# Performance work log

Measured on AMD Instinct MI355X. Metric: run time of the kernel, lower is better.

## Reference

```python
import jax, jax.numpy as jnp
import numpy as np


def setup_inputs() -> dict:
    key = jax.random.key(0)
    ks = jax.random.split(key, 9)
    B, Cr, H, W = 16, 1024, 28, 28
    Cs, Hs, Ws = 256, 25, 25  # Hs == Ws so adaptive pool == mean over width
    Ci = 512
    return {
        "x_rgb": jax.random.normal(ks[0], (B, Cr, H, W), jnp.float32),
        "x_skel": jax.random.normal(ks[1], (B, Cs, Hs, Ws), jnp.float32),
        "Wq": jax.random.normal(ks[2], (Ci, Cr), jnp.float32) * (Cr ** -0.5),
        "bq": jax.random.normal(ks[3], (Ci,), jnp.float32) * 0.01,
        "Wk": jax.random.normal(ks[4], (Ci, Cs), jnp.float32) * (Cs ** -0.5),
        "bk": jax.random.normal(ks[5], (Ci,), jnp.float32) * 0.01,
        "Wv": jax.random.normal(ks[6], (Cr, Cs), jnp.float32) * (Cs ** -0.5),
        "bv": jax.random.normal(ks[7], (Cr,), jnp.float32) * 0.01,
        "gamma": jax.random.normal(ks[8], (1,), jnp.float32) * 0.1,
    }


def reference(x_rgb, x_skel, Wq, bq, Wk, bk, Wv, bv, gamma):
    B, Cr, H, W = x_rgb.shape
    Ws = x_skel.shape[3]
    # adaptive_avg_pool2d(x_skel, (Ws, 1)) with Hs == Ws -> mean over width
    pooled = jnp.mean(x_skel, axis=3)  # [B, Cs, Ws]
    # 1x1 conv projections as matmuls
    q = jnp.einsum('ic,bchw->bihw', Wq, x_rgb) + bq[None, :, None, None]
    q = q.reshape(B, -1, H * W).transpose(0, 2, 1)          # [B, HW, Ci]
    k = jnp.einsum('ic,bcs->bis', Wk, pooled) + bk[None, :, None]  # [B, Ci, Ws]
    energy = jnp.einsum('bni,bis->bns', q, k)               # [B, HW, Ws]
    attention = jax.nn.softmax(energy, axis=-1)             # [B, HW, Ws]
    v = jnp.einsum('rc,bcs->brs', Wv, pooled) + bv[None, :, None]  # [B, Cr, Ws]
    out = jnp.einsum('brs,bns->brn', v, attention)          # [B, Cr, HW]
    out = out.reshape(B, Cr, H, W)
    return gamma[0] * out + x_rgb
```

## Files before the change

### kernel.cpp

```cpp
#include <hip/hip_runtime.h>

#define BB 16
#define CR 1024
#define HWD 784
#define HW2 392
#define CS 256
#define SSZ 25
#define SP 28
#define CI 512
#define CSPLIT 8
#define CCHUNK 128
#define RSPLIT 16
#define RCHUNK 64

#define OFF_POOLED 0
#define OFF_GB     102400
#define OFF_H      103424
#define OFF_VP     103680
#define OFF_MP     562432
#define OFF_E0     1021184
#define OFF_ATT    1021584
#define OFF_EPG    1335184

__global__ __launch_bounds__(256) void k_G(const float* __restrict__ Wq,
                                           const float* __restrict__ Wk,
                                           float* __restrict__ G) {
    int cp = threadIdx.x;
    int c0 = blockIdx.x * 4;
    float a0 = 0.f, a1 = 0.f, a2 = 0.f, a3 = 0.f;
#pragma unroll 4
    for (int i = 0; i < CI; ++i) {
        float wk = Wk[(size_t)i * CS + cp];
        float4 wq = *(const float4*)(Wq + (size_t)i * CR + c0);
        a0 = fmaf(wq.x, wk, a0);
        a1 = fmaf(wq.y, wk, a1);
        a2 = fmaf(wq.z, wk, a2);
        a3 = fmaf(wq.w, wk, a3);
    }
    G[(size_t)(c0 + 0) * CS + cp] = a0;
    G[(size_t)(c0 + 1) * CS + cp] = a1;
    G[(size_t)(c0 + 2) * CS + cp] = a2;
    G[(size_t)(c0 + 3) * CS + cp] = a3;
}

__global__ __launch_bounds__(256) void k_bias(const float* __restrict__ Wq,
                                              const float* __restrict__ Wk,
                                              const float* __restrict__ bq,
                                              const float* __restrict__ bk,
                                              float* __restrict__ gb,
                                              float* __restrict__ h) {
    if (blockIdx.x < 4) {
        int c = blockIdx.x * 256 + threadIdx.x;
        float a = 0.f;
        for (int i = 0; i < CI; ++i) a = fmaf(Wq[(size_t)i * CR + c], bk[i], a);
        gb[c] = a;
    } else {
        int cp = threadIdx.x;
        float a = 0.f;
        for (int i = 0; i < CI; ++i) a = fmaf(Wk[(size_t)i * CS + cp], bq[i], a);
        h[cp] = a;
    }
}

__global__ __launch_bounds__(256) void k_pool(const float* __restrict__ xs,
                                              float* __restrict__ pooled) {
    __shared__ float buf[4][400];
    int wave = threadIdx.x >> 6, lane = threadIdx.x & 63;
    int r0 = blockIdx.x * 64 + wave * 16;
    const float4* src = (const float4*)(xs + (size_t)r0 * SSZ);
    float4* b4 = (float4*)buf[wave];
    b4[lane] = src[lane];
    if (lane < 36) b4[64 + lane] = src[64 + lane];
    __syncthreads();
    if (lane < 16) {
        const float* row = buf[wave] + lane * SSZ;
        float s = 0.f;
#pragma unroll
        for (int w = 0; w < SSZ; ++w) s += row[w];
        pooled[r0 + lane] = s * (1.0f / SSZ);
    }
}

template <int NS>
__device__ __forceinline__ void proj_body(const float* __restrict__ wrow,
                                          const float* __restrict__ pb, int s0,
                                          float bias, float* __restrict__ dst,
                                          bool zpad) {
    float acc[NS];
#pragma unroll
    for (int i = 0; i < NS; ++i) acc[i] = 0.f;
    const float4* w4 = (const float4*)wrow;
#pragma unroll 2
    for (int c4 = 0; c4 < CS / 4; ++c4) {
        float4 w = w4[c4];
        const float* p = pb + c4 * 4 * SSZ + s0;
#pragma unroll
        for (int i = 0; i < NS; ++i)
            acc[i] = fmaf(w.x, p[i],
                     fmaf(w.y, p[SSZ + i],
                     fmaf(w.z, p[2 * SSZ + i],
                     fmaf(w.w, p[3 * SSZ + i], acc[i]))));
    }
#pragma unroll
    for (int i = 0; i < NS; ++i) dst[s0 + i] = acc[i] + bias;
    if (zpad) { dst[25] = 0.f; dst[26] = 0.f; dst[27] = 0.f; }
}

__global__ __launch_bounds__(256) void k_proj(const float* __restrict__ G,
                                              const float* __restrict__ Wv,
                                              const float* __restrict__ gb,
                                              const float* __restrict__ bv,
                                              const float* __restrict__ pooled,
                                              float* __restrict__ Mp,
                                              float* __restrict__ vp) {
    int q = blockIdx.x, b = blockIdx.y;
    int which = q & 1, cblk = (q >> 1) & 3, sh = q >> 3;
    int row = cblk * 256 + threadIdx.x;
    const float* pb = pooled + (size_t)b * CS * SSZ;
    const float* wrow = (which ? Wv : G) + (size_t)row * CS;
    float bias = which ? bv[row] : gb[row];
    float* dst = (which ? vp : Mp) + ((size_t)b * CR + row) * SP;
    if (sh == 0) proj_body<13>(wrow, pb, 0, bias, dst, false);
    else         proj_body<12>(wrow, pb, 13, bias, dst, true);
}

__global__ __launch_bounds__(256) void k_e0(const float* __restrict__ h,
                                            const float* __restrict__ bq,
                                            const float* __restrict__ bk,
                                            const float* __restrict__ pooled,
                                            float* __restrict__ e0) {
    int t = blockIdx.x * 256 + threadIdx.x;
    if (t >= BB * SSZ) return;
    int b = t / SSZ, s = t % SSZ;
    float a = 0.f;
    for (int i = 0; i < CI; ++i) a = fmaf(bq[i], bk[i], a);
    const float* pb = pooled + (size_t)b * CS * SSZ + s;
    for (int cp = 0; cp < CS; ++cp) a = fmaf(h[cp], pb[cp * SSZ], a);
    e0[t] = a;
}

__global__ __launch_bounds__(64) void k_energy(const float* __restrict__ xr,
                                               const float* __restrict__ Mp,
                                               float* __restrict__ Ep) {
    __shared__ float ldsM[CCHUNK * SP];
    int lane = threadIdx.x;
    int b = blockIdx.y, ch = blockIdx.z;
    int cbeg = ch * CCHUNK;
    {
        const float4* src = (const float4*)(Mp + ((size_t)b * CR + cbeg) * SP);
        float4* dst = (float4*)ldsM;
#pragma unroll
        for (int j = 0; j < 14; ++j) dst[lane + 64 * j] = src[lane + 64 * j];
    }
    __syncthreads();

    int n2 = blockIdx.x * 64 + lane;
    bool valid = n2 < HW2;
    int n2c = valid ? n2 : 0;
    const float2* x2 = (const float2*)(xr + (size_t)b * CR * HWD);

    float acc0[SP], acc1[SP];
#pragma unroll
    for (int s = 0; s < SP; ++s) { acc0[s] = 0.f; acc1[s] = 0.f; }

#pragma unroll 2
    for (int c = 0; c < CCHUNK; ++c) {
        float2 xv = x2[(size_t)(cbeg + c) * HW2 + n2c];
        const float4* mr = (const float4*)&ldsM[c * SP];
#pragma unroll
        for (int j = 0; j < 7; ++j) {
            float4 m = mr[j];
            acc0[4 * j + 0] = fmaf(xv.x, m.x, acc0[4 * j + 0]);
            acc0[4 * j + 1] = fmaf(xv.x, m.y, acc0[4 * j + 1]);
            acc0[4 * j + 2] = fmaf(xv.x, m.z, acc0[4 * j + 2]);
            acc0[4 * j + 3] = fmaf(xv.x, m.w, acc0[4 * j + 3]);
            acc1[4 * j + 0] = fmaf(xv.y, m.x, acc1[4 * j + 0]);
            acc1[4 * j + 1] = fmaf(xv.y, m.y, acc1[4 * j + 1]);
            acc1[4 * j + 2] = fmaf(xv.y, m.z, acc1[4 * j + 2]);
            acc1[4 * j + 3] = fmaf(xv.y, m.w, acc1[4 * j + 3]);
        }
    }
    if (valid) {
        float2* ep = (float2*)Ep + ((size_t)(ch * BB + b) * SSZ) * HW2 + n2;
#pragma unroll
        for (int s = 0; s < SSZ; ++s) ep[(size_t)s * HW2] = make_float2(acc0[s], acc1[s]);
    }
}

__global__ __launch_bounds__(64) void k_softmax(const float* __restrict__ Ep,
                                                const float* __restrict__ e0,
                                                float* __restrict__ att) {
    int lane = threadIdx.x;
    int n2 = blockIdx.x * 64 + lane;
    int b = blockIdx.y;
    if (n2 >= HW2) return;
    float ex[SSZ], ey[SSZ];
#pragma unroll
    for (int s = 0; s < SSZ; ++s) { float v = e0[b * SSZ + s]; ex[s] = v; ey[s] = v; }
    const float2* ep2 = (const float2*)Ep;
    for (int ch = 0; ch < CSPLIT; ++ch) {
        const float2* ep = ep2 + ((size_t)(ch * BB + b) * SSZ) * HW2 + n2;
#pragma unroll
        for (int s = 0; s < SSZ; ++s) {
            float2 v = ep[(size_t)s * HW2];
            ex[s] += v.x; ey[s] += v.y;
        }
    }
    float mx = ex[0], my = ey[0];
#pragma unroll
    for (int s = 1; s < SSZ; ++s) { mx = fmaxf(mx, ex[s]); my = fmaxf(my, ey[s]); }
    float sx = 0.f, sy = 0.f;
#pragma unroll
    for (int s = 0; s < SSZ; ++s) {
        ex[s] = __expf(ex[s] - mx); sx += ex[s];
        ey[s] = __expf(ey[s] - my); sy += ey[s];
    }
    float ix = 1.0f / sx, iy = 1.0f / sy;
    float2* ao = (float2*)att + ((size_t)b * SSZ) * HW2 + n2;
#pragma unroll
    for (int s = 0; s < SSZ; ++s) ao[(size_t)s * HW2] = make_float2(ex[s] * ix, ey[s] * iy);
}

__global__ __launch_bounds__(64) void k_out(const float* __restrict__ xr,
                                            const float* __restrict__ vp,
                                            const float* __restrict__ att,
                                            const float* __restrict__ gamma,
                                            float* __restrict__ out) {
    __shared__ float ldsv[RCHUNK * SP];
    int lane = threadIdx.x;
    int b = blockIdx.y, rz = blockIdx.z;
    int r0 = rz * RCHUNK;
    {
        const float4* src = (const float4*)(vp + ((size_t)b * CR + r0) * SP);
        float4* dst = (float4*)ldsv;
#pragma unroll
        for (int j = 0; j < 7; ++j) dst[lane + 64 * j] = src[lane + 64 * j];
    }
    __syncthreads();

    int n2 = blockIdx.x * 64 + lane;
    bool valid = n2 < HW2;
    int n2c = valid ? n2 : 0;

    float a0[SP], a1[SP];
    const float2* at2 = (const float2*)att + ((size_t)b * SSZ) * HW2 + n2c;
#pragma unroll
    for (int s = 0; s < SSZ; ++s) {
        float2 av = at2[(size_t)s * HW2];
        a0[s] = av.x; a1[s] = av.y;
    }
#pragma unroll
    for (int s = SSZ; s < SP; ++s) { a0[s] = 0.f; a1[s] = 0.f; }

    float g = gamma[0];
    const float2* x2 = (const float2*)(xr + (size_t)b * CR * HWD);
    float2* o2 = (float2*)(out + (size_t)b * CR * HWD);

#pragma unroll 2
    for (int r = 0; r < RCHUNK; ++r) {
        float d0 = 0.f, d1 = 0.f;
        const float4* vr = (const float4*)&ldsv[r * SP];
#pragma unroll
        for (int j = 0; j < 7; ++j) {
            float4 v = vr[j];
            d0 = fmaf(v.x, a0[4 * j + 0], d0);
            d0 = fmaf(v.y, a0[4 * j + 1], d0);
            d0 = fmaf(v.z, a0[4 * j + 2], d0);
            d0 = fmaf(v.w, a0[4 * j + 3], d0);
            d1 = fmaf(v.x, a1[4 * j + 0], d1);
            d1 = fmaf(v.y, a1[4 * j + 1], d1);
            d1 = fmaf(v.z, a1[4 * j + 2], d1);
            d1 = fmaf(v.w, a1[4 * j + 3], d1);
        }
        float2 xv = x2[(size_t)(r0 + r) * HW2 + n2c];
        if (valid)
            o2[(size_t)(r0 + r) * HW2 + n2] = make_float2(fmaf(g, d0, xv.x), fmaf(g, d1, xv.y));
    }
}

extern "C" void kernel_launch(void* const* d_in, const int* in_sizes, int n_in,
                              void* d_out, int out_size, void* d_ws, size_t ws_size,
                              hipStream_t stream) {
    const float* x_rgb  = (const float*)d_in[0];
    const float* x_skel = (const float*)d_in[1];
    const float* Wq     = (const float*)d_in[2];
    const float* bq     = (const float*)d_in[3];
    const float* Wk     = (const float*)d_in[4];
    const float* bk     = (const float*)d_in[5];
    const float* Wv     = (const float*)d_in[6];
    const float* bv     = (const float*)d_in[7];
    const float* gamma  = (const float*)d_in[8];
    float* out = (float*)d_out;

    float* ws     = (float*)d_ws;
    float* pooled = ws + OFF_POOLED;
    float* gb     = ws + OFF_GB;
    float* h      = ws + OFF_H;
    float* vp     = ws + OFF_VP;
    float* Mp     = ws + OFF_MP;
    float* e0     = ws + OFF_E0;
    float* att    = ws + OFF_ATT;
    float* Ep     = ws + OFF_EPG;
    float* G      = ws + OFF_EPG;

    k_G      <<<dim3(256),            256, 0, stream>>>(Wq, Wk, G);
    k_bias   <<<dim3(5),              256, 0, stream>>>(Wq, Wk, bq, bk, gb, h);
    k_pool   <<<dim3(1600),           256, 0, stream>>>(x_skel, pooled);
    k_proj   <<<dim3(16, 16),         256, 0, stream>>>(G, Wv, gb, bv, pooled, Mp, vp);
    k_e0     <<<dim3(2),              256, 0, stream>>>(h, bq, bk, pooled, e0);
    k_energy <<<dim3(7, 16, CSPLIT),   64, 0, stream>>>(x_rgb, Mp, Ep);
    k_softmax<<<dim3(7, 16),           64, 0, stream>>>(Ep, e0, att);
    k_out    <<<dim3(7, 16, RSPLIT),   64, 0, stream>>>(x_rgb, vp, att, gamma, out);
}
```

Before: 282.1 us.

## Compute K per batch first, then Wq^T K, replacing precomputed Wq^T Wk product

Changes the association of the energy product. Instead of forming G = Wq^T Wk (1024x256 over CI=512) plus separate bias kernels, the code now projects pooled features to k (including bk) per batch, then forms M = Wq^T k per batch, and computes e0 from bq·k. This removes the k_G and k_bias kernels. In exchange it adds per-batch work over CI. It also unrolls x loads in the energy loop, halves the row chunk in k_out (doubling its blocks), hoists the residual load, and raises unroll factors.

```diff
diff --git a/kernel.cpp b/kernel.cpp
--- a/kernel.cpp
+++ b/kernel.cpp
@@ -10,57 +10,15 @@
 #define CI 512
 #define CSPLIT 8
 #define CCHUNK 128
-#define RSPLIT 16
-#define RCHUNK 64
+#define RSPLIT 32
+#define RCHUNK 32
 
 #define OFF_POOLED 0
-#define OFF_GB     102400
-#define OFF_H      103424
-#define OFF_VP     103680
-#define OFF_MP     562432
-#define OFF_E0     1021184
-#define OFF_ATT    1021584
-#define OFF_EPG    1335184
-
-__global__ __launch_bounds__(256) void k_G(const float* __restrict__ Wq,
-                                           const float* __restrict__ Wk,
-                                           float* __restrict__ G) {
-    int cp = threadIdx.x;
-    int c0 = blockIdx.x * 4;
-    float a0 = 0.f, a1 = 0.f, a2 = 0.f, a3 = 0.f;
-#pragma unroll 4
-    for (int i = 0; i < CI; ++i) {
-        float wk = Wk[(size_t)i * CS + cp];
-        float4 wq = *(const float4*)(Wq + (size_t)i * CR + c0);
-        a0 = fmaf(wq.x, wk, a0);
-        a1 = fmaf(wq.y, wk, a1);
-        a2 = fmaf(wq.z, wk, a2);
-        a3 = fmaf(wq.w, wk, a3);
-    }
-    G[(size_t)(c0 + 0) * CS + cp] = a0;
-    G[(size_t)(c0 + 1) * CS + cp] = a1;
-    G[(size_t)(c0 + 2) * CS + cp] = a2;
-    G[(size_t)(c0 + 3) * CS + cp] = a3;
-}
-
-__global__ __launch_bounds__(256) void k_bias(const float* __restrict__ Wq,
-                                              const float* __restrict__ Wk,
-                                              const float* __restrict__ bq,
-                                              const float* __restrict__ bk,
-                                              float* __restrict__ gb,
-                                              float* __restrict__ h) {
-    if (blockIdx.x < 4) {
-        int c = blockIdx.x * 256 + threadIdx.x;
-        float a = 0.f;
-        for (int i = 0; i < CI; ++i) a = fmaf(Wq[(size_t)i * CR + c], bk[i], a);
-        gb[c] = a;
-    } else {
-        int cp = threadIdx.x;
-        float a = 0.f;
-        for (int i = 0; i < CI; ++i) a = fmaf(Wk[(size_t)i * CS + cp], bq[i], a);
-        h[cp] = a;
-    }
-}
+#define OFF_VP     102400
+#define OFF_MP     561152
+#define OFF_E0     1019904
+#define OFF_ATT    1020304
+#define OFF_EP     1333904
 
 __global__ __launch_bounds__(256) void k_pool(const float* __restrict__ xs,
                                               float* __restrict__ pooled) {
@@ -90,7 +48,7 @@
 #pragma unroll
     for (int i = 0; i < NS; ++i) acc[i] = 0.f;
     const float4* w4 = (const float4*)wrow;
-#pragma unroll 2
+#pragma unroll 4
     for (int c4 = 0; c4 < CS / 4; ++c4) {
         float4 w = w4[c4];
         const float* p = pb + c4 * 4 * SSZ + s0;
@@ -106,36 +64,77 @@
     if (zpad) { dst[25] = 0.f; dst[26] = 0.f; dst[27] = 0.f; }
 }
 
-__global__ __launch_bounds__(256) void k_proj(const float* __restrict__ G,
-                                              const float* __restrict__ Wv,
-                                              const float* __restrict__ gb,
-                                              const float* __restrict__ bv,
-                                              const float* __restrict__ pooled,
-                                              float* __restrict__ Mp,
-                                              float* __restrict__ vp) {
-    int q = blockIdx.x, b = blockIdx.y;
-    int which = q & 1, cblk = (q >> 1) & 3, sh = q >> 3;
-    int row = cblk * 256 + threadIdx.x;
+__global__ __launch_bounds__(256) void k_kkv(const float* __restrict__ Wk,
+                                             const float* __restrict__ Wv,
+                                             const float* __restrict__ bk,
+                                             const float* __restrict__ bv,
+                                             const float* __restrict__ pooled,
+                                             float* __restrict__ kk,
+                                             float* __restrict__ vp) {
+    int rb = blockIdx.x >> 2, sh = blockIdx.x & 3;
+    int b = blockIdx.y;
     const float* pb = pooled + (size_t)b * CS * SSZ;
-    const float* wrow = (which ? Wv : G) + (size_t)row * CS;
-    float bias = which ? bv[row] : gb[row];
-    float* dst = (which ? vp : Mp) + ((size_t)b * CR + row) * SP;
-    if (sh == 0) proj_body<13>(wrow, pb, 0, bias, dst, false);
-    else         proj_body<12>(wrow, pb, 13, bias, dst, true);
-}
-
-__global__ __launch_bounds__(256) void k_e0(const float* __restrict__ h,
-                                            const float* __restrict__ bq,
-                                            const float* __restrict__ bk,
-                                            const float* __restrict__ pooled,
+    const float* wrow;
+    float bias;
+    float* dst;
+    if (rb < 2) {
+        int i = rb * 256 + threadIdx.x;
+        wrow = Wk + (size_t)i * CS;
+        bias = bk[i];
+        dst = kk + ((size_t)b * CI + i) * SP;
+    } else {
+        int r = (rb - 2) * 256 + threadIdx.x;
+        wrow = Wv + (size_t)r * CS;
+        bias = bv[r];
+        dst = vp + ((size_t)b * CR + r) * SP;
+    }
+    int s0 = sh * 7;
+    if (sh < 3) proj_body<7>(wrow, pb, s0, bias, dst, false);
+    else        proj_body<4>(wrow, pb, s0, bias, dst, true);
+}
+
+template <int NS>
+__device__ __forceinline__ void m_body(const float* __restrict__ Wq,
+                                       const float* __restrict__ kkb, int c, int s0,
+                                       float* __restrict__ dst, bool zpad) {
+    float acc[NS];
+#pragma unroll
+    for (int i = 0; i < NS; ++i) acc[i] = 0.f;
+#pragma unroll 4
+    for (int i = 0; i < CI; ++i) {
+        float w = Wq[(size_t)i * CR + c];
+        const float* kr = kkb + i * SP + s0;
+#pragma unroll
+        for (int j = 0; j < NS; ++j) acc[j] = fmaf(w, kr[j], acc[j]);
+    }
+#pragma unroll
+    for (int j = 0; j < NS; ++j) dst[s0 + j] = acc[j];
+    if (zpad) { dst[25] = 0.f; dst[26] = 0.f; dst[27] = 0.f; }
+}
+
+__global__ __launch_bounds__(256) void k_M(const float* __restrict__ Wq,
+                                           const float* __restrict__ kk,
+                                           float* __restrict__ Mp) {
+    int cblk = blockIdx.x >> 2, sh = blockIdx.x & 3;
+    int b = blockIdx.y;
+    int c = cblk * 256 + threadIdx.x;
+    const float* kkb = kk + (size_t)b * CI * SP;
+    float* dst = Mp + ((size_t)b * CR + c) * SP;
+    int s0 = sh * 7;
+    if (sh < 3) m_body<7>(Wq, kkb, c, s0, dst, false);
+    else        m_body<4>(Wq, kkb, c, s0, dst, true);
+}
+
+__global__ __launch_bounds__(256) void k_e0(const float* __restrict__ bq,
+                                            const float* __restrict__ kk,
                                             float* __restrict__ e0) {
     int t = blockIdx.x * 256 + threadIdx.x;
     if (t >= BB * SSZ) return;
     int b = t / SSZ, s = t % SSZ;
+    const float* kb = kk + (size_t)b * CI * SP + s;
     float a = 0.f;
-    for (int i = 0; i < CI; ++i) a = fmaf(bq[i], bk[i], a);
-    const float* pb = pooled + (size_t)b * CS * SSZ + s;
-    for (int cp = 0; cp < CS; ++cp) a = fmaf(h[cp], pb[cp * SSZ], a);
+#pragma unroll 4
+    for (int i = 0; i < CI; ++i) a = fmaf(bq[i], kb[(size_t)i * SP], a);
     e0[t] = a;
 }
 
@@ -163,21 +162,26 @@
 #pragma unroll
     for (int s = 0; s < SP; ++s) { acc0[s] = 0.f; acc1[s] = 0.f; }
 
-#pragma unroll 2
-    for (int c = 0; c < CCHUNK; ++c) {
-        float2 xv = x2[(size_t)(cbeg + c) * HW2 + n2c];
-        const float4* mr = (const float4*)&ldsM[c * SP];
-#pragma unroll
-        for (int j = 0; j < 7; ++j) {
-            float4 m = mr[j];
-            acc0[4 * j + 0] = fmaf(xv.x, m.x, acc0[4 * j + 0]);
-            acc0[4 * j + 1] = fmaf(xv.x, m.y, acc0[4 * j + 1]);
-            acc0[4 * j + 2] = fmaf(xv.x, m.z, acc0[4 * j + 2]);
-            acc0[4 * j + 3] = fmaf(xv.x, m.w, acc0[4 * j + 3]);
-            acc1[4 * j + 0] = fmaf(xv.y, m.x, acc1[4 * j + 0]);
-            acc1[4 * j + 1] = fmaf(xv.y, m.y, acc1[4 * j + 1]);
-            acc1[4 * j + 2] = fmaf(xv.y, m.z, acc1[4 * j + 2]);
-            acc1[4 * j + 3] = fmaf(xv.y, m.w, acc1[4 * j + 3]);
+    for (int c = 0; c < CCHUNK; c += 4) {
+        float2 xv[4];
+#pragma unroll
+        for (int u = 0; u < 4; ++u)
+            xv[u] = x2[(size_t)(cbeg + c + u) * HW2 + n2c];
+#pragma unroll
+        for (int u = 0; u < 4; ++u) {
+            const float4* mr = (const float4*)&ldsM[(c + u) * SP];
+#pragma unroll
+            for (int j = 0; j < 7; ++j) {
+                float4 m = mr[j];
+                acc0[4 * j + 0] = fmaf(xv[u].x, m.x, acc0[4 * j + 0]);
+                acc0[4 * j + 1] = fmaf(xv[u].x, m.y, acc0[4 * j + 1]);
+                acc0[4 * j + 2] = fmaf(xv[u].x, m.z, acc0[4 * j + 2]);
+                acc0[4 * j + 3] = fmaf(xv[u].x, m.w, acc0[4 * j + 3]);
+                acc1[4 * j + 0] = fmaf(xv[u].y, m.x, acc1[4 * j + 0]);
+                acc1[4 * j + 1] = fmaf(xv[u].y, m.y, acc1[4 * j + 1]);
+                acc1[4 * j + 2] = fmaf(xv[u].y, m.z, acc1[4 * j + 2]);
+                acc1[4 * j + 3] = fmaf(xv[u].y, m.w, acc1[4 * j + 3]);
+            }
         }
     }
     if (valid) {
@@ -234,7 +238,10 @@
         const float4* src = (const float4*)(vp + ((size_t)b * CR + r0) * SP);
         float4* dst = (float4*)ldsv;
 #pragma unroll
-        for (int j = 0; j < 7; ++j) dst[lane + 64 * j] = src[lane + 64 * j];
+        for (int j = 0; j < 4; ++j) {
+            int idx = lane + 64 * j;
+            if (idx < RCHUNK * SP / 4) dst[idx] = src[idx];
+        }
     }
     __syncthreads();
 
@@ -256,8 +263,9 @@
     const float2* x2 = (const float2*)(xr + (size_t)b * CR * HWD);
     float2* o2 = (float2*)(out + (size_t)b * CR * HWD);
 
-#pragma unroll 2
+#pragma unroll 4
     for (int r = 0; r < RCHUNK; ++r) {
+        float2 xv = x2[(size_t)(r0 + r) * HW2 + n2c];
         float d0 = 0.f, d1 = 0.f;
         const float4* vr = (const float4*)&ldsv[r * SP];
 #pragma unroll
@@ -272,7 +280,6 @@
             d1 = fmaf(v.z, a1[4 * j + 2], d1);
             d1 = fmaf(v.w, a1[4 * j + 3], d1);
         }
-        float2 xv = x2[(size_t)(r0 + r) * HW2 + n2c];
         if (valid)
             o2[(size_t)(r0 + r) * HW2 + n2] = make_float2(fmaf(g, d0, xv.x), fmaf(g, d1, xv.y));
     }
@@ -294,20 +301,17 @@
 
     float* ws     = (float*)d_ws;
     float* pooled = ws + OFF_POOLED;
-    float* gb     = ws + OFF_GB;
-    float* h      = ws + OFF_H;
     float* vp     = ws + OFF_VP;
     float* Mp     = ws + OFF_MP;
     float* e0     = ws + OFF_E0;
     float* att    = ws + OFF_ATT;
-    float* Ep     = ws + OFF_EPG;
-    float* G      = ws + OFF_EPG;
-
-    k_G      <<<dim3(256),            256, 0, stream>>>(Wq, Wk, G);
-    k_bias   <<<dim3(5),              256, 0, stream>>>(Wq, Wk, bq, bk, gb, h);
+    float* Ep     = ws + OFF_EP;
+    float* kk     = ws + OFF_EP;
+
     k_pool   <<<dim3(1600),           256, 0, stream>>>(x_skel, pooled);
-    k_proj   <<<dim3(16, 16),         256, 0, stream>>>(G, Wv, gb, bv, pooled, Mp, vp);
-    k_e0     <<<dim3(2),              256, 0, stream>>>(h, bq, bk, pooled, e0);
+    k_kkv    <<<dim3(24, 16),         256, 0, stream>>>(Wk, Wv, bk, bv, pooled, kk, vp);
+    k_M      <<<dim3(16, 16),         256, 0, stream>>>(Wq, kk, Mp);
+    k_e0     <<<dim3(2),              256, 0, stream>>>(bq, kk, e0);
     k_energy <<<dim3(7, 16, CSPLIT),   64, 0, stream>>>(x_rgb, Mp, Ep);
     k_softmax<<<dim3(7, 16),           64, 0, stream>>>(Ep, e0, att);
     k_out    <<<dim3(7, 16, RSPLIT),   64, 0, stream>>>(x_rgb, vp, att, gamma, out);
```

After: 300.3 us. 1.06x slower.
